# Performance work log

Hardware: AMD Instinct MI355X
Metric: run time of the kernel (lower is better)

## Reference

```python
import jax, jax.numpy as jnp
import numpy as np

N_E = 8192
E_DIM = 256
BETA = 0.25
SIGMA = 0.1


def setup_inputs() -> dict:
    key = jax.random.key(0)
    kz, ke = jax.random.split(key)
    z = jax.random.normal(kz, (16, 256, 32, 32), dtype=jnp.float32)
    # torch init: uniform(-1/n_e, 1/n_e)
    emb = jax.random.uniform(ke, (N_E, E_DIM), minval=-1.0 / N_E, maxval=1.0 / N_E, dtype=jnp.float32)
    return {"z": z, "emb": emb}


def _vq_forward(z, emb, beta=BETA, sigma=SIGMA):
    b, c, h, w = z.shape  # c == e_dim
    z_bhwc = jnp.transpose(z, (0, 2, 3, 1))  # b h w c
    zf = z_bhwc.reshape(-1, c)  # [b*h*w, c]

    # d[i, n] = ||zf_i||^2 + ||e_n||^2 - 2 zf_i . e_n
    e2 = jnp.sum(emb ** 2, axis=1)  # [n_e]
    d = jnp.sum(zf ** 2, axis=1, keepdims=True) + e2 - 2.0 * (zf @ emb.T)  # [bhw, n_e]

    # codebook-codebook pairwise distances
    d1 = e2[:, None] + e2[None, :] - 2.0 * (emb @ emb.T)  # [n_e, n_e]
    # torch.kthvalue(d1, 2, 0): 2nd smallest along dim 0, per column
    min_dist = jnp.sort(d1, axis=0)[1]  # [n_e]
    total_min_distance = jnp.sum(min_dist)
    codebookvariance = jnp.std(min_dist, ddof=1)  # torch.std is unbiased

    min_encoding_indices = jnp.argmin(d, axis=1)  # [bhw]
    # d[range, argmin] == row-wise min
    distances = jnp.min(d, axis=1).reshape(b, h, w)
    # rbf: exp(-(d^2).mean(axis=1) / (2*sigma^2)) -> [b, w]
    distances = jnp.exp(-jnp.mean(distances ** 2, axis=1) / (2.0 * sigma ** 2))

    z_q = jnp.take(emb, min_encoding_indices, axis=0).reshape(b, h, w, c)

    sg = jax.lax.stop_gradient
    # legacy=True branch
    loss = (jnp.mean((sg(z_q) - z_bhwc) ** 2)
            + beta * jnp.mean((z_q - sg(z_bhwc)) ** 2)
            - total_min_distance)

    # straight-through estimator
    z_q = z_bhwc + sg(z_q - z_bhwc)
    z_q_bchw = jnp.transpose(z_q, (0, 3, 1, 2))  # b c h w (contiguous)
    # torch .view(b, h*w, e_dim) on contiguous bchw buffer: raw reshape
    z_flattened1 = z_q_bchw.reshape(b, h * w, c)

    return (z_q_bchw, loss, distances, min_encoding_indices,
            z_flattened1, codebookvariance, total_min_distance)


def reference(z, emb):
    return _vq_forward(z, emb)
```

## Files before the change

kernel.cpp:

```cpp
#include <hip/hip_runtime.h>
#include <stdint.h>

#define N_E   8192
#define EDIM  256
#define NB    16
#define HH    32
#define WW    32
#define HW    1024
#define NI    16384
#define NELEM 4194304

#define MARGIN    2.5e-4f
#define MARGIN_D1 2e-8f
#define ITEM_CAP  262144

#define O_ZQ   0
#define O_LOSS 4194304
#define O_DIST 4194305
#define O_IDX  4194817
#define O_ZFL  4211201
#define O_CBV  8405505
#define O_TMD  8405506

#define WS_PMIN  0
#define WS_IDX   131072
#define WS_DMIN  196608
#define WS_E2    262144
#define WS_Z2    294912
#define WS_MSE   360448
#define WS_CNT   360456
#define WS_MIND  360512
#define WS_ZA    1048576
#define WS_EB    9437184
#define WS_M     13631488
#define WS_ITEMS 30408704

typedef __attribute__((ext_vector_type(8))) short bf16x8;
typedef __attribute__((ext_vector_type(4))) float f32x4;

__device__ __forceinline__ short f2bf(float f) {
    unsigned u = __float_as_uint(f);
    u += 0x7fffu + ((u >> 16) & 1u);
    return (short)(u >> 16);
}

__global__ void k_init(unsigned long long* __restrict__ pmin, double* __restrict__ mse,
                       int* __restrict__ cnt) {
    int t = blockIdx.x * 256 + threadIdx.x;
    if (t < NI) pmin[t] = 0xFFFFFFFFFFFFFFFFull;
    if (t == 0) { *mse = 0.0; *cnt = 0; }
}

__global__ void k_e2(const float* __restrict__ emb, float* __restrict__ e2) {
    int row  = blockIdx.x * 4 + (threadIdx.x >> 6);
    int lane = threadIdx.x & 63;
    float4 v = *reinterpret_cast<const float4*>(emb + (size_t)row * EDIM + lane * 4);
    float s = v.x * v.x + v.y * v.y + v.z * v.z + v.w * v.w;
    #pragma unroll
    for (int m = 32; m; m >>= 1) s += __shfl_xor(s, m);
    if (lane == 0) e2[row] = s;
}

__global__ void k_z2(const float* __restrict__ z, float* __restrict__ z2) {
    int i = blockIdx.x * 256 + threadIdx.x;
    int b = i >> 10, hw = i & 1023;
    const float* p = z + (size_t)b * EDIM * HW + hw;
    float s = 0.f;
    #pragma unroll 8
    for (int c = 0; c < EDIM; ++c) { float v = p[(size_t)c * HW]; s += v * v; }
    z2[i] = s;
}

__global__ void k_convert_z(const float* __restrict__ z, bf16x8* __restrict__ zA) {
    __shared__ float lds[64][65];
    const int t   = threadIdx.x;
    const int hw0 = blockIdx.x * 64;
    const int c0  = blockIdx.y * 64;
    const int b   = blockIdx.z;
    #pragma unroll
    for (int cc = 0; cc < 4; ++cc) {
        const int cl = cc * 16 + (t >> 4);
        const float4 v = *reinterpret_cast<const float4*>(
            z + ((size_t)(b * 256 + c0 + cl) << 10) + hw0 + (t & 15) * 4);
        lds[cl][(t & 15) * 4 + 0] = v.x; lds[cl][(t & 15) * 4 + 1] = v.y;
        lds[cl][(t & 15) * 4 + 2] = v.z; lds[cl][(t & 15) * 4 + 3] = v.w;
    }
    __syncthreads();
    const int hl = t & 63;
    const int i  = b * 1024 + hw0 + hl;
    const int ig = i >> 4, r = i & 15;
    #pragma unroll
    for (int half = 0; half < 2; ++half) {
        const int kqi = (t >> 6) + half * 4;
        const int kq  = (c0 >> 3) + kqi;
        bf16x8 o;
        #pragma unroll
        for (int j = 0; j < 8; ++j) o[j] = f2bf(lds[kqi * 8 + j][hl]);
        zA[(ig * 32 + kq) * 16 + r] = o;
    }
}

__global__ void k_convert_e(const float* __restrict__ emb, bf16x8* __restrict__ eB) {
    const int t  = threadIdx.x;
    const int kq = t & 31;
    const int n  = blockIdx.x * 8 + (t >> 5);
    const float4 u = *reinterpret_cast<const float4*>(emb + (size_t)n * EDIM + kq * 8);
    const float4 v = *reinterpret_cast<const float4*>(emb + (size_t)n * EDIM + kq * 8 + 4);
    bf16x8 o;
    o[0] = f2bf(u.x); o[1] = f2bf(u.y); o[2] = f2bf(u.z); o[3] = f2bf(u.w);
    o[4] = f2bf(v.x); o[5] = f2bf(v.y); o[6] = f2bf(v.z); o[7] = f2bf(v.w);
    eB[((n >> 4) * 32 + kq) * 16 + (n & 15)] = o;
}

__launch_bounds__(256, 2)
__global__ void k_cand(const bf16x8* __restrict__ zA, const bf16x8* __restrict__ eB,
                       const float* __restrict__ e2, float* __restrict__ m) {
    const int t = threadIdx.x;
    const int w = t >> 6, l = t & 63;
    const int lo16 = l & 15, hi4 = l >> 4;
    const int iblk = blockIdx.x, chunk = blockIdx.y;
    const int ig0 = (iblk * 128 + w * 32) >> 4;

    bf16x8 a[2][8];
    #pragma unroll
    for (int ig = 0; ig < 2; ++ig)
        #pragma unroll
        for (int st = 0; st < 8; ++st)
            a[ig][st] = zA[((ig0 + ig) * 32 + st * 4 + hi4) * 16 + lo16];

    for (int ns = 0; ns < 8; ++ns) {
        const int n0 = chunk * 1024 + ns * 128;
        f32x4 acc[2][8];
        #pragma unroll
        for (int ig = 0; ig < 2; ++ig)
            #pragma unroll
            for (int cg = 0; cg < 8; ++cg) acc[ig][cg] = (f32x4){0.f, 0.f, 0.f, 0.f};
        float e2v[8];
        #pragma unroll
        for (int cg = 0; cg < 8; ++cg) e2v[cg] = e2[n0 + cg * 16 + lo16];

        #pragma unroll
        for (int st = 0; st < 8; ++st) {
            #pragma unroll
            for (int cg = 0; cg < 8; ++cg) {
                const bf16x8 b = eB[(((n0 >> 4) + cg) * 32 + st * 4 + hi4) * 16 + lo16];
                acc[0][cg] = __builtin_amdgcn_mfma_f32_16x16x32_bf16(a[0][st], b, acc[0][cg], 0, 0, 0);
                acc[1][cg] = __builtin_amdgcn_mfma_f32_16x16x32_bf16(a[1][st], b, acc[1][cg], 0, 0, 0);
            }
        }
        #pragma unroll
        for (int ig = 0; ig < 2; ++ig) {
            #pragma unroll
            for (int reg = 0; reg < 4; ++reg) {
                const int row = iblk * 128 + w * 32 + ig * 16 + hi4 * 4 + reg;
                #pragma unroll
                for (int gp = 0; gp < 4; ++gp) {
                    float v = fminf(fmaf(-2.f, acc[ig][2 * gp][reg],     e2v[2 * gp]),
                                    fmaf(-2.f, acc[ig][2 * gp + 1][reg], e2v[2 * gp + 1]));
                    v = fminf(v, __shfl_xor(v, 1));
                    v = fminf(v, __shfl_xor(v, 2));
                    v = fminf(v, __shfl_xor(v, 4));
                    v = fminf(v, __shfl_xor(v, 8));
                    if (lo16 == gp) m[row * 256 + chunk * 32 + ns * 4 + gp] = v;
                }
            }
        }
    }
}

__launch_bounds__(256, 2)
__global__ void k_cand_d1(const bf16x8* __restrict__ eB, const float* __restrict__ e2,
                          float* __restrict__ md1) {
    const int t = threadIdx.x;
    const int w = t >> 6, l = t & 63;
    const int lo16 = l & 15, hi4 = l >> 4;
    const int iblk = blockIdx.x, chunk = blockIdx.y;
    const int ig0 = (iblk * 128 + w * 32) >> 4;

    bf16x8 a[2][8];
    #pragma unroll
    for (int ig = 0; ig < 2; ++ig)
        #pragma unroll
        for (int st = 0; st < 8; ++st)
            a[ig][st] = eB[((ig0 + ig) * 32 + st * 4 + hi4) * 16 + lo16];

    for (int ns = 0; ns < 8; ++ns) {
        const int n0 = chunk * 1024 + ns * 128;
        f32x4 acc[2][8];
        #pragma unroll
        for (int ig = 0; ig < 2; ++ig)
            #pragma unroll
            for (int cg = 0; cg < 8; ++cg) acc[ig][cg] = (f32x4){0.f, 0.f, 0.f, 0.f};
        float e2v[8];
        #pragma unroll
        for (int cg = 0; cg < 8; ++cg) e2v[cg] = e2[n0 + cg * 16 + lo16];

        #pragma unroll
        for (int st = 0; st < 8; ++st) {
            #pragma unroll
            for (int cg = 0; cg < 8; ++cg) {
                const bf16x8 b = eB[(((n0 >> 4) + cg) * 32 + st * 4 + hi4) * 16 + lo16];
                acc[0][cg] = __builtin_amdgcn_mfma_f32_16x16x32_bf16(a[0][st], b, acc[0][cg], 0, 0, 0);
                acc[1][cg] = __builtin_amdgcn_mfma_f32_16x16x32_bf16(a[1][st], b, acc[1][cg], 0, 0, 0);
            }
        }
        #pragma unroll
        for (int ig = 0; ig < 2; ++ig) {
            #pragma unroll
            for (int reg = 0; reg < 4; ++reg) {
                const int row = iblk * 128 + w * 32 + ig * 16 + hi4 * 4 + reg;
                #pragma unroll
                for (int gp = 0; gp < 4; ++gp) {
                    float v = fminf(fmaf(-2.f, acc[ig][2 * gp][reg],     e2v[2 * gp]),
                                    fmaf(-2.f, acc[ig][2 * gp + 1][reg], e2v[2 * gp + 1]));
                    v = fminf(v, __shfl_xor(v, 1));
                    v = fminf(v, __shfl_xor(v, 2));
                    v = fminf(v, __shfl_xor(v, 4));
                    v = fminf(v, __shfl_xor(v, 8));
                    if (lo16 == gp) md1[row * 256 + chunk * 32 + ns * 4 + gp] = v;
                }
            }
        }
    }
}

__global__ void k_select(const float* __restrict__ m, int* __restrict__ cnt,
                         unsigned* __restrict__ items) {
    const int t = threadIdx.x;
    const int row = blockIdx.x * 4 + (t >> 6);
    const int l = t & 63;
    const float4 mv = reinterpret_cast<const float4*>(m + (size_t)row * 256)[l];
    float v = fminf(fminf(mv.x, mv.y), fminf(mv.z, mv.w));
    #pragma unroll
    for (int o = 32; o; o >>= 1) v = fminf(v, __shfl_xor(v, o));
    const float thr = v + MARGIN;
    if (mv.x <= thr) { int p = atomicAdd(cnt, 1); if (p < ITEM_CAP) items[p] = (row << 8) | (l * 4 + 0); }
    if (mv.y <= thr) { int p = atomicAdd(cnt, 1); if (p < ITEM_CAP) items[p] = (row << 8) | (l * 4 + 1); }
    if (mv.z <= thr) { int p = atomicAdd(cnt, 1); if (p < ITEM_CAP) items[p] = (row << 8) | (l * 4 + 2); }
    if (mv.w <= thr) { int p = atomicAdd(cnt, 1); if (p < ITEM_CAP) items[p] = (row << 8) | (l * 4 + 3); }
}

__global__ void k_rescore(const float* __restrict__ z, const float* __restrict__ emb,
                          const float* __restrict__ z2, const float* __restrict__ e2,
                          const int* __restrict__ cnt, const unsigned* __restrict__ items,
                          unsigned long long* __restrict__ pmin) {
    const int t = threadIdx.x;
    const int l = t & 63;
    const int wid = blockIdx.x * 4 + (t >> 6);
    int n_items = *cnt; if (n_items > ITEM_CAP) n_items = ITEM_CAP;
    for (int it = wid; it < n_items; it += 16384) {
        const unsigned item = items[it];
        const int row = item >> 8, g = item & 255;
        const int n = g * 32 + (l & 31);
        const int half = l >> 5;
        const float* zp = z + ((size_t)(row >> 10) << 18) + (row & 1023) + (size_t)(half * 128) * HW;
        const float* ep = emb + (size_t)n * EDIM + half * 128;
        float acc = 0.f;
        #pragma unroll 8
        for (int c = 0; c < 128; ++c) acc = fmaf(zp[(size_t)c * HW], ep[c], acc);
        acc += __shfl_xor(acc, 32);
        const float t0 = z2[row] + e2[n];
        const float d  = fmaf(-2.f, acc, t0);
        unsigned long long pk = ((unsigned long long)__float_as_uint(d) << 32) | (unsigned)n;
        #pragma unroll
        for (int o = 1; o < 64; o <<= 1) {
            const unsigned long long op = __shfl_xor(pk, o);
            if (op < pk) pk = op;
        }
        if (l == 0) atomicMin(&pmin[row], pk);
    }
}

__global__ void k_d1_final(const float* __restrict__ emb, const float* __restrict__ e2,
                           const float* __restrict__ md1, float* __restrict__ mind) {
    const int t = threadIdx.x, l = t & 63;
    const int n = blockIdx.x * 4 + (t >> 6);
    const float4 mv = reinterpret_cast<const float4*>(md1 + (size_t)n * 256)[l];
    const float lo1 = fminf(mv.x, mv.y), hi1 = fmaxf(mv.x, mv.y);
    const float lo2 = fminf(mv.z, mv.w), hi2 = fmaxf(mv.z, mv.w);
    float a1 = fminf(lo1, lo2);
    float a2 = fminf(fmaxf(lo1, lo2), fminf(hi1, hi2));
    #pragma unroll
    for (int o = 1; o < 64; o <<= 1) {
        const float o1 = __shfl_xor(a1, o), o2 = __shfl_xor(a2, o);
        const float n1 = fminf(a1, o1);
        const float n2 = fminf(fmaxf(a1, o1), fminf(a2, o2));
        a1 = n1; a2 = n2;
    }
    const float thr = a2 + MARGIN_D1;
    const float e2n = e2[n];
    const float* np = emb + (size_t)n * EDIM;
    float b1 = 3.4e38f, b2 = 3.4e38f;
    const float slot[4] = {mv.x, mv.y, mv.z, mv.w};
    #pragma unroll
    for (int s = 0; s < 4; ++s) {
        unsigned long long mask = __ballot(slot[s] <= thr);
        while (mask) {
            const int src = __builtin_ctzll(mask); mask &= mask - 1;
            const int g = src * 4 + s;
            const int mm = g * 32 + (l & 31);
            const float* ep = emb + (size_t)mm * EDIM;
            float acc = 0.f;
            #pragma unroll 8
            for (int c = 0; c < EDIM; ++c) acc = fmaf(ep[c], np[c], acc);
            float dv = (e2[mm] + e2n) - 2.0f * acc;
            if (l >= 32) dv = 3.4e38f;
            if (dv < b1) { b2 = b1; b1 = dv; }
            else if (dv < b2) { b2 = dv; }
        }
    }
    #pragma unroll
    for (int o = 1; o < 64; o <<= 1) {
        const float o1 = __shfl_xor(b1, o), o2 = __shfl_xor(b2, o);
        const float n1 = fminf(b1, o1);
        const float n2 = fminf(fmaxf(b1, o1), fminf(b2, o2));
        b1 = n1; b2 = n2;
    }
    if (l == 0) mind[n] = b2;
}

__global__ void k_unpack(const unsigned long long* __restrict__ pmin,
                         int* __restrict__ idxi, float* __restrict__ dmin,
                         float* __restrict__ out_idx) {
    int i = blockIdx.x * 256 + threadIdx.x;
    unsigned long long p = pmin[i];
    int idx  = (int)(p & 0xFFFFFFFFull);
    idxi[i]  = idx;
    dmin[i]  = __uint_as_float((unsigned)(p >> 32));
    out_idx[i] = (float)idx;
}

__global__ void k_epilogue(const float* __restrict__ z, const float* __restrict__ emb,
                           const int* __restrict__ idxi,
                           float* __restrict__ out_zq, float* __restrict__ out_zfl,
                           double* __restrict__ mse) {
    const int j4 = blockIdx.x * 256 + threadIdx.x;
    const int j  = j4 * 4;
    const int b  = j >> 18;
    const int c  = (j >> 10) & 255;
    const int hw = j & 1023;
    const int ib = (b << 10) + hw;
    const float4 zv = *reinterpret_cast<const float4*>(z + j);
    const float q0 = emb[(size_t)idxi[ib + 0] * EDIM + c];
    const float q1 = emb[(size_t)idxi[ib + 1] * EDIM + c];
    const float q2 = emb[(size_t)idxi[ib + 2] * EDIM + c];
    const float q3 = emb[(size_t)idxi[ib + 3] * EDIM + c];
    const float d0 = q0 - zv.x, d1 = q1 - zv.y, d2 = q2 - zv.z, d3 = q3 - zv.w;
    const float4 st = {zv.x + d0, zv.y + d1, zv.z + d2, zv.w + d3};
    *reinterpret_cast<float4*>(out_zq + j) = st;
    out_zfl[j + 0] = st.x; out_zfl[j + 1] = st.y; out_zfl[j + 2] = st.z; out_zfl[j + 3] = st.w;

    double s = (double)(d0 * d0) + (double)(d1 * d1) + (double)(d2 * d2) + (double)(d3 * d3);
    #pragma unroll
    for (int m = 32; m; m >>= 1) s += __shfl_down(s, m);
    __shared__ double part[4];
    if ((threadIdx.x & 63) == 0) part[threadIdx.x >> 6] = s;
    __syncthreads();
    if (threadIdx.x == 0) atomicAdd(mse, part[0] + part[1] + part[2] + part[3]);
}

__global__ void k_distances(const float* __restrict__ dmin, float* __restrict__ out_d) {
    int t = threadIdx.x;
    int b = t >> 5, w = t & 31;
    float s = 0.f;
    #pragma unroll
    for (int h = 0; h < HH; ++h) {
        float d = dmin[(b << 10) + (h << 5) + w];
        s += d * d;
    }
    float mean = s * (1.0f / 32.0f);
    out_d[t] = expf(-mean / 0.02f);
}

__global__ void k_finalize(const float* __restrict__ mind, const double* __restrict__ mse,
                           float* __restrict__ out) {
    const int t = threadIdx.x;
    double s = 0.0, ss = 0.0;
    for (int n = t; n < N_E; n += 256) {
        const double v = (double)mind[n];
        s += v; ss += v * v;
    }
    #pragma unroll
    for (int m = 32; m; m >>= 1) { s += __shfl_down(s, m); ss += __shfl_down(ss, m); }
    __shared__ double rs[4], rss[4];
    if ((t & 63) == 0) { rs[t >> 6] = s; rss[t >> 6] = ss; }
    __syncthreads();
    if (t == 0) {
        const double S  = rs[0] + rs[1] + rs[2] + rs[3];
        const double SS = rss[0] + rss[1] + rss[2] + rss[3];
        const float tmd = (float)S;
        double var = (SS - S * S / (double)N_E) / (double)(N_E - 1);
        if (var < 0.0) var = 0.0;
        const float cbv = (float)sqrt(var);
        const float m1  = (float)(*mse / (double)NELEM);
        const float lossf = m1 + 0.25f * m1 - tmd;
        out[O_LOSS] = lossf;
        out[O_CBV]  = cbv;
        out[O_TMD]  = tmd;
    }
}

extern "C" void kernel_launch(void* const* d_in, const int* in_sizes, int n_in,
                              void* d_out, int out_size, void* d_ws, size_t ws_size,
                              hipStream_t stream) {
    const float* z   = (const float*)d_in[0];
    const float* emb = (const float*)d_in[1];
    float* out = (float*)d_out;
    char*  ws  = (char*)d_ws;

    unsigned long long* pmin = (unsigned long long*)(ws + WS_PMIN);
    int*      idxi  = (int*)    (ws + WS_IDX);
    float*    dmin  = (float*)  (ws + WS_DMIN);
    float*    e2    = (float*)  (ws + WS_E2);
    float*    z2    = (float*)  (ws + WS_Z2);
    double*   mse   = (double*) (ws + WS_MSE);
    int*      cnt   = (int*)    (ws + WS_CNT);
    float*    mind  = (float*)  (ws + WS_MIND);
    bf16x8*   zA    = (bf16x8*) (ws + WS_ZA);
    bf16x8*   eB    = (bf16x8*) (ws + WS_EB);
    float*    marr  = (float*)  (ws + WS_M);
    unsigned* items = (unsigned*)(ws + WS_ITEMS);

    k_init     <<<64,   256, 0, stream>>>(pmin, mse, cnt);
    k_e2       <<<2048, 256, 0, stream>>>(emb, e2);
    k_z2       <<<64,   256, 0, stream>>>(z, z2);
    k_convert_z<<<dim3(16, 4, 16), 256, 0, stream>>>(z, zA);
    k_convert_e<<<1024, 256, 0, stream>>>(emb, eB);
    k_cand     <<<dim3(128, 8), 256, 0, stream>>>(zA, eB, e2, marr);
    k_select   <<<4096, 256, 0, stream>>>(marr, cnt, items);
    k_rescore  <<<4096, 256, 0, stream>>>(z, emb, z2, e2, cnt, items, pmin);
    k_cand_d1  <<<dim3(64, 8), 256, 0, stream>>>(eB, e2, marr);
    k_d1_final <<<2048, 256, 0, stream>>>(emb, e2, marr, mind);
    k_unpack   <<<64,   256, 0, stream>>>(pmin, idxi, dmin, out + O_IDX);
    k_epilogue <<<4096, 256, 0, stream>>>(z, emb, idxi, out + O_ZQ, out + O_ZFL, mse);
    k_distances<<<1,    512, 0, stream>>>(dmin, out + O_DIST);
    k_finalize <<<1,    256, 0, stream>>>(mind, mse, out);
}
```

Before: 1.165 ms.

## Coarsen candidate groups to 128 codes and rescore per row without atomics

The bf16 candidate kernels now reduce each 128-code group to a single min, so the candidate array shrinks from 256 to 64 floats per row. The separate select kernel, its global atomic counter and the item list are removed. A per-row wavefront thresholds its own groups with a ballot and rescores each selected group exactly in fp32, two codes per lane, then writes the row minimum directly, dropping the atomicMin and the pmin initialisation. The codebook second-nearest pass is restructured the same way with a widened margin. Coarser groups mean each selected group costs more exact FP32 work and more groups may pass the threshold, trading extra rescoring for fewer launches, less memory traffic and no atomics.

```diff
diff --git a/kernel.cpp b/kernel.cpp
--- a/kernel.cpp
+++ b/kernel.cpp
@@ -12,7 +12,6 @@
 
 #define MARGIN    2.5e-4f
 #define MARGIN_D1 2e-8f
-#define ITEM_CAP  262144
 
 #define O_ZQ   0
 #define O_LOSS 4194304
@@ -28,12 +27,11 @@
 #define WS_E2    262144
 #define WS_Z2    294912
 #define WS_MSE   360448
-#define WS_CNT   360456
 #define WS_MIND  360512
 #define WS_ZA    1048576
 #define WS_EB    9437184
-#define WS_M     13631488
-#define WS_ITEMS 30408704
+#define WS_M128  13631488
+#define WS_MD1   17825792
 
 typedef __attribute__((ext_vector_type(8))) short bf16x8;
 typedef __attribute__((ext_vector_type(4))) float f32x4;
@@ -44,11 +42,8 @@
     return (short)(u >> 16);
 }
 
-__global__ void k_init(unsigned long long* __restrict__ pmin, double* __restrict__ mse,
-                       int* __restrict__ cnt) {
-    int t = blockIdx.x * 256 + threadIdx.x;
-    if (t < NI) pmin[t] = 0xFFFFFFFFFFFFFFFFull;
-    if (t == 0) { *mse = 0.0; *cnt = 0; }
+__global__ void k_init(double* __restrict__ mse) {
+    if (threadIdx.x == 0) *mse = 0.0;
 }
 
 __global__ void k_e2(const float* __restrict__ emb, float* __restrict__ e2) {
@@ -114,7 +109,7 @@
 
 __launch_bounds__(256, 2)
 __global__ void k_cand(const bf16x8* __restrict__ zA, const bf16x8* __restrict__ eB,
-                       const float* __restrict__ e2, float* __restrict__ m) {
+                       const float* __restrict__ e2, float* __restrict__ m128) {
     const int t = threadIdx.x;
     const int w = t >> 6, l = t & 63;
     const int lo16 = l & 15, hi4 = l >> 4;
@@ -152,16 +147,17 @@
         for (int ig = 0; ig < 2; ++ig) {
             #pragma unroll
             for (int reg = 0; reg < 4; ++reg) {
-                const int row = iblk * 128 + w * 32 + ig * 16 + hi4 * 4 + reg;
+                float v = fmaf(-2.f, acc[ig][0][reg], e2v[0]);
                 #pragma unroll
-                for (int gp = 0; gp < 4; ++gp) {
-                    float v = fminf(fmaf(-2.f, acc[ig][2 * gp][reg],     e2v[2 * gp]),
-                                    fmaf(-2.f, acc[ig][2 * gp + 1][reg], e2v[2 * gp + 1]));
-                    v = fminf(v, __shfl_xor(v, 1));
-                    v = fminf(v, __shfl_xor(v, 2));
-                    v = fminf(v, __shfl_xor(v, 4));
-                    v = fminf(v, __shfl_xor(v, 8));
-                    if (lo16 == gp) m[row * 256 + chunk * 32 + ns * 4 + gp] = v;
+                for (int cg = 1; cg < 8; ++cg)
+                    v = fminf(v, fmaf(-2.f, acc[ig][cg][reg], e2v[cg]));
+                v = fminf(v, __shfl_xor(v, 1));
+                v = fminf(v, __shfl_xor(v, 2));
+                v = fminf(v, __shfl_xor(v, 4));
+                v = fminf(v, __shfl_xor(v, 8));
+                if (lo16 == ns) {
+                    const int row = iblk * 128 + w * 32 + ig * 16 + hi4 * 4 + reg;
+                    m128[row * 64 + chunk * 8 + ns] = v;
                 }
             }
         }
@@ -208,78 +204,79 @@
         for (int ig = 0; ig < 2; ++ig) {
             #pragma unroll
             for (int reg = 0; reg < 4; ++reg) {
-                const int row = iblk * 128 + w * 32 + ig * 16 + hi4 * 4 + reg;
+                float v = fmaf(-2.f, acc[ig][0][reg], e2v[0]);
                 #pragma unroll
-                for (int gp = 0; gp < 4; ++gp) {
-                    float v = fminf(fmaf(-2.f, acc[ig][2 * gp][reg],     e2v[2 * gp]),
-                                    fmaf(-2.f, acc[ig][2 * gp + 1][reg], e2v[2 * gp + 1]));
-                    v = fminf(v, __shfl_xor(v, 1));
-                    v = fminf(v, __shfl_xor(v, 2));
-                    v = fminf(v, __shfl_xor(v, 4));
-                    v = fminf(v, __shfl_xor(v, 8));
-                    if (lo16 == gp) md1[row * 256 + chunk * 32 + ns * 4 + gp] = v;
+                for (int cg = 1; cg < 8; ++cg)
+                    v = fminf(v, fmaf(-2.f, acc[ig][cg][reg], e2v[cg]));
+                v = fminf(v, __shfl_xor(v, 1));
+                v = fminf(v, __shfl_xor(v, 2));
+                v = fminf(v, __shfl_xor(v, 4));
+                v = fminf(v, __shfl_xor(v, 8));
+                if (lo16 == ns) {
+                    const int row = iblk * 128 + w * 32 + ig * 16 + hi4 * 4 + reg;
+                    md1[row * 64 + chunk * 8 + ns] = v;
                 }
             }
         }
     }
 }
 
-__global__ void k_select(const float* __restrict__ m, int* __restrict__ cnt,
-                         unsigned* __restrict__ items) {
-    const int t = threadIdx.x;
+__global__ void k_rescore_row(const float* __restrict__ z, const float* __restrict__ emb,
+                              const float* __restrict__ z2, const float* __restrict__ e2,
+                              const float* __restrict__ m128,
+                              unsigned long long* __restrict__ pmin) {
+    const int t = threadIdx.x, l = t & 63;
     const int row = blockIdx.x * 4 + (t >> 6);
-    const int l = t & 63;
-    const float4 mv = reinterpret_cast<const float4*>(m + (size_t)row * 256)[l];
-    float v = fminf(fminf(mv.x, mv.y), fminf(mv.z, mv.w));
-    #pragma unroll
-    for (int o = 32; o; o >>= 1) v = fminf(v, __shfl_xor(v, o));
-    const float thr = v + MARGIN;
-    if (mv.x <= thr) { int p = atomicAdd(cnt, 1); if (p < ITEM_CAP) items[p] = (row << 8) | (l * 4 + 0); }
-    if (mv.y <= thr) { int p = atomicAdd(cnt, 1); if (p < ITEM_CAP) items[p] = (row << 8) | (l * 4 + 1); }
-    if (mv.z <= thr) { int p = atomicAdd(cnt, 1); if (p < ITEM_CAP) items[p] = (row << 8) | (l * 4 + 2); }
-    if (mv.w <= thr) { int p = atomicAdd(cnt, 1); if (p < ITEM_CAP) items[p] = (row << 8) | (l * 4 + 3); }
-}
-
-__global__ void k_rescore(const float* __restrict__ z, const float* __restrict__ emb,
-                          const float* __restrict__ z2, const float* __restrict__ e2,
-                          const int* __restrict__ cnt, const unsigned* __restrict__ items,
-                          unsigned long long* __restrict__ pmin) {
-    const int t = threadIdx.x;
-    const int l = t & 63;
-    const int wid = blockIdx.x * 4 + (t >> 6);
-    int n_items = *cnt; if (n_items > ITEM_CAP) n_items = ITEM_CAP;
-    for (int it = wid; it < n_items; it += 16384) {
-        const unsigned item = items[it];
-        const int row = item >> 8, g = item & 255;
-        const int n = g * 32 + (l & 31);
-        const int half = l >> 5;
-        const float* zp = z + ((size_t)(row >> 10) << 18) + (row & 1023) + (size_t)(half * 128) * HW;
-        const float* ep = emb + (size_t)n * EDIM + half * 128;
-        float acc = 0.f;
-        #pragma unroll 8
-        for (int c = 0; c < 128; ++c) acc = fmaf(zp[(size_t)c * HW], ep[c], acc);
-        acc += __shfl_xor(acc, 32);
-        const float t0 = z2[row] + e2[n];
-        const float d  = fmaf(-2.f, acc, t0);
-        unsigned long long pk = ((unsigned long long)__float_as_uint(d) << 32) | (unsigned)n;
-        #pragma unroll
-        for (int o = 1; o < 64; o <<= 1) {
-            const unsigned long long op = __shfl_xor(pk, o);
-            if (op < pk) pk = op;
-        }
-        if (l == 0) atomicMin(&pmin[row], pk);
-    }
+    const float v = m128[row * 64 + l];
+    float mn = v;
+    #pragma unroll
+    for (int o = 1; o < 64; o <<= 1) mn = fminf(mn, __shfl_xor(mn, o));
+    unsigned long long mm = __ballot(v <= mn + MARGIN);
+
+    const float* zp = z + ((size_t)(row >> 10) << 18) + (row & 1023);
+    const float z2r = z2[row];
+    unsigned long long best = 0xFFFFFFFFFFFFFFFFull;
+    while (mm) {
+        const int g = __builtin_ctzll(mm); mm &= mm - 1;
+        const int n = g * 128 + l * 2;
+        const float* ep0 = emb + (size_t)n * EDIM;
+        const float* ep1 = ep0 + EDIM;
+        float a0l = 0.f, a0h = 0.f, a1l = 0.f, a1h = 0.f;
+        #pragma unroll 4
+        for (int c = 0; c < 128; ++c) {
+            const float zc = zp[(size_t)c << 10];
+            a0l = fmaf(zc, ep0[c], a0l);
+            a1l = fmaf(zc, ep1[c], a1l);
+        }
+        #pragma unroll 4
+        for (int c = 128; c < 256; ++c) {
+            const float zc = zp[(size_t)c << 10];
+            a0h = fmaf(zc, ep0[c], a0h);
+            a1h = fmaf(zc, ep1[c], a1h);
+        }
+        const float d0 = fmaf(-2.f, a0l + a0h, z2r + e2[n]);
+        const float d1 = fmaf(-2.f, a1l + a1h, z2r + e2[n + 1]);
+        const unsigned long long p0 =
+            ((unsigned long long)__float_as_uint(d0) << 32) | (unsigned)n;
+        const unsigned long long p1 =
+            ((unsigned long long)__float_as_uint(d1) << 32) | (unsigned)(n + 1);
+        const unsigned long long pl = p0 < p1 ? p0 : p1;
+        if (pl < best) best = pl;
+    }
+    #pragma unroll
+    for (int o = 1; o < 64; o <<= 1) {
+        const unsigned long long ob = __shfl_xor(best, o);
+        if (ob < best) best = ob;
+    }
+    if (l == 0) pmin[row] = best;
 }
 
 __global__ void k_d1_final(const float* __restrict__ emb, const float* __restrict__ e2,
                            const float* __restrict__ md1, float* __restrict__ mind) {
     const int t = threadIdx.x, l = t & 63;
     const int n = blockIdx.x * 4 + (t >> 6);
-    const float4 mv = reinterpret_cast<const float4*>(md1 + (size_t)n * 256)[l];
-    const float lo1 = fminf(mv.x, mv.y), hi1 = fmaxf(mv.x, mv.y);
-    const float lo2 = fminf(mv.z, mv.w), hi2 = fmaxf(mv.z, mv.w);
-    float a1 = fminf(lo1, lo2);
-    float a2 = fminf(fmaxf(lo1, lo2), fminf(hi1, hi2));
+    const float v = md1[n * 64 + l];
+    float a1 = v, a2 = 3.4e38f;
     #pragma unroll
     for (int o = 1; o < 64; o <<= 1) {
         const float o1 = __shfl_xor(a1, o), o2 = __shfl_xor(a2, o);
@@ -287,27 +284,29 @@
         const float n2 = fminf(fmaxf(a1, o1), fminf(a2, o2));
         a1 = n1; a2 = n2;
     }
-    const float thr = a2 + MARGIN_D1;
+    const float thr = a2 + 2.0f * MARGIN_D1;
+    unsigned long long mm = __ballot(v <= thr);
     const float e2n = e2[n];
     const float* np = emb + (size_t)n * EDIM;
     float b1 = 3.4e38f, b2 = 3.4e38f;
-    const float slot[4] = {mv.x, mv.y, mv.z, mv.w};
-    #pragma unroll
-    for (int s = 0; s < 4; ++s) {
-        unsigned long long mask = __ballot(slot[s] <= thr);
-        while (mask) {
-            const int src = __builtin_ctzll(mask); mask &= mask - 1;
-            const int g = src * 4 + s;
-            const int mm = g * 32 + (l & 31);
-            const float* ep = emb + (size_t)mm * EDIM;
-            float acc = 0.f;
-            #pragma unroll 8
-            for (int c = 0; c < EDIM; ++c) acc = fmaf(ep[c], np[c], acc);
-            float dv = (e2[mm] + e2n) - 2.0f * acc;
-            if (l >= 32) dv = 3.4e38f;
-            if (dv < b1) { b2 = b1; b1 = dv; }
-            else if (dv < b2) { b2 = dv; }
-        }
+    while (mm) {
+        const int g = __builtin_ctzll(mm); mm &= mm - 1;
+        const int m0 = g * 128 + l * 2;
+        const float* p0 = emb + (size_t)m0 * EDIM;
+        const float* p1 = p0 + EDIM;
+        float c0 = 0.f, c1 = 0.f;
+        #pragma unroll 8
+        for (int c = 0; c < EDIM; ++c) {
+            const float nc = np[c];
+            c0 = fmaf(p0[c], nc, c0);
+            c1 = fmaf(p1[c], nc, c1);
+        }
+        const float d0 = (e2[m0] + e2n) - 2.0f * c0;
+        const float d1 = (e2[m0 + 1] + e2n) - 2.0f * c1;
+        const float lo = fminf(d0, d1), hi = fmaxf(d0, d1);
+        const float nb1 = fminf(b1, lo);
+        const float nb2 = fminf(fmaxf(b1, lo), fminf(b2, hi));
+        b1 = nb1; b2 = nb2;
     }
     #pragma unroll
     for (int o = 1; o < 64; o <<= 1) {
@@ -414,25 +413,23 @@
     float*    e2    = (float*)  (ws + WS_E2);
     float*    z2    = (float*)  (ws + WS_Z2);
     double*   mse   = (double*) (ws + WS_MSE);
-    int*      cnt   = (int*)    (ws + WS_CNT);
     float*    mind  = (float*)  (ws + WS_MIND);
     bf16x8*   zA    = (bf16x8*) (ws + WS_ZA);
     bf16x8*   eB    = (bf16x8*) (ws + WS_EB);
-    float*    marr  = (float*)  (ws + WS_M);
-    unsigned* items = (unsigned*)(ws + WS_ITEMS);
-
-    k_init     <<<64,   256, 0, stream>>>(pmin, mse, cnt);
-    k_e2       <<<2048, 256, 0, stream>>>(emb, e2);
-    k_z2       <<<64,   256, 0, stream>>>(z, z2);
-    k_convert_z<<<dim3(16, 4, 16), 256, 0, stream>>>(z, zA);
-    k_convert_e<<<1024, 256, 0, stream>>>(emb, eB);
-    k_cand     <<<dim3(128, 8), 256, 0, stream>>>(zA, eB, e2, marr);
-    k_select   <<<4096, 256, 0, stream>>>(marr, cnt, items);
-    k_rescore  <<<4096, 256, 0, stream>>>(z, emb, z2, e2, cnt, items, pmin);
-    k_cand_d1  <<<dim3(64, 8), 256, 0, stream>>>(eB, e2, marr);
-    k_d1_final <<<2048, 256, 0, stream>>>(emb, e2, marr, mind);
-    k_unpack   <<<64,   256, 0, stream>>>(pmin, idxi, dmin, out + O_IDX);
-    k_epilogue <<<4096, 256, 0, stream>>>(z, emb, idxi, out + O_ZQ, out + O_ZFL, mse);
-    k_distances<<<1,    512, 0, stream>>>(dmin, out + O_DIST);
-    k_finalize <<<1,    256, 0, stream>>>(mind, mse, out);
-}
+    float*    m128  = (float*)  (ws + WS_M128);
+    float*    md1   = (float*)  (ws + WS_MD1);
+
+    k_init       <<<1,    64,  0, stream>>>(mse);
+    k_e2         <<<2048, 256, 0, stream>>>(emb, e2);
+    k_z2         <<<64,   256, 0, stream>>>(z, z2);
+    k_convert_z  <<<dim3(16, 4, 16), 256, 0, stream>>>(z, zA);
+    k_convert_e  <<<1024, 256, 0, stream>>>(emb, eB);
+    k_cand       <<<dim3(128, 8), 256, 0, stream>>>(zA, eB, e2, m128);
+    k_rescore_row<<<4096, 256, 0, stream>>>(z, emb, z2, e2, m128, pmin);
+    k_cand_d1    <<<dim3(64, 8), 256, 0, stream>>>(eB, e2, md1);
+    k_d1_final   <<<2048, 256, 0, stream>>>(emb, e2, md1, mind);
+    k_unpack     <<<64,   256, 0, stream>>>(pmin, idxi, dmin, out + O_IDX);
+    k_epilogue   <<<4096, 256, 0, stream>>>(z, emb, idxi, out + O_ZQ, out + O_ZFL, mse);
+    k_distances  <<<1,    512, 0, stream>>>(dmin, out + O_DIST);
+    k_finalize   <<<1,    256, 0, stream>>>(mind, mse, out);
+}
```

Measured after the change: 2.155 ms. +85.0%, slower.

## Use split-bf16 triple MFMA with in-kernel top-2 tracking, drop select/rescore passes

Applied to the files above, without the earlier changes.

Both GEMM kernels now split each fp32 operand into bf16 high and low parts and issue three MFMAs (hi*hi, hi*lo, lo*hi) per tile, giving near-fp32 accuracy. Each thread tracks a packed (distance key, index) top-2 per row in registers and writes only two candidates per row per chunk, instead of dumping per-group minima. The atomic-based select and rescore pipeline is replaced by small merge kernels that rescore just the top-2 candidates exactly in fp32. This cuts candidate-buffer traffic and atomics, and the A fragments are now reloaded per step instead of held in registers. The cost is three times the MFMA work, and the reduced candidate set relies on the split-bf16 precision to keep the true minimum.

```diff
diff --git a/kernel.cpp b/kernel.cpp
--- a/kernel.cpp
+++ b/kernel.cpp
@@ -10,9 +10,7 @@
 #define NI    16384
 #define NELEM 4194304
 
-#define MARGIN    2.5e-4f
-#define MARGIN_D1 2e-8f
-#define ITEM_CAP  262144
+#define MARGIN_D1 1e-9f
 
 #define O_ZQ   0
 #define O_LOSS 4194304
@@ -22,18 +20,18 @@
 #define O_CBV  8405505
 #define O_TMD  8405506
 
-#define WS_PMIN  0
-#define WS_IDX   131072
-#define WS_DMIN  196608
-#define WS_E2    262144
-#define WS_Z2    294912
-#define WS_MSE   360448
-#define WS_CNT   360456
-#define WS_MIND  360512
-#define WS_ZA    1048576
-#define WS_EB    9437184
-#define WS_M     13631488
-#define WS_ITEMS 30408704
+#define WS_IDX   0x0
+#define WS_DMIN  0x20000
+#define WS_E2    0x40000
+#define WS_Z2    0x50000
+#define WS_MSE   0x60000
+#define WS_MIND  0x61000
+#define WS_PZ    0x70000
+#define WS_PD1   0x270000
+#define WS_ZAH   0x400000
+#define WS_ZAL   0xC00000
+#define WS_EBH   0x1400000
+#define WS_EBL   0x1800000
 
 typedef __attribute__((ext_vector_type(8))) short bf16x8;
 typedef __attribute__((ext_vector_type(4))) float f32x4;
@@ -43,12 +41,30 @@
     u += 0x7fffu + ((u >> 16) & 1u);
     return (short)(u >> 16);
 }
-
-__global__ void k_init(unsigned long long* __restrict__ pmin, double* __restrict__ mse,
-                       int* __restrict__ cnt) {
-    int t = blockIdx.x * 256 + threadIdx.x;
-    if (t < NI) pmin[t] = 0xFFFFFFFFFFFFFFFFull;
-    if (t == 0) { *mse = 0.0; *cnt = 0; }
+__device__ __forceinline__ float bf2f(short h) {
+    return __uint_as_float(((unsigned)(unsigned short)h) << 16);
+}
+__device__ __forceinline__ unsigned keyf(float f) {
+    unsigned b = __float_as_uint(f);
+    return (b & 0x80000000u) ? ~b : (b | 0x80000000u);
+}
+__device__ __forceinline__ float unkeyf(unsigned k) {
+    return (k & 0x80000000u) ? __uint_as_float(k ^ 0x80000000u) : __uint_as_float(~k);
+}
+__device__ __forceinline__ void ins2(unsigned long long& a1, unsigned long long& a2,
+                                     unsigned long long v) {
+    if (v < a1) { a2 = a1; a1 = v; } else if (v < a2) { a2 = v; }
+}
+__device__ __forceinline__ void mrg2(unsigned long long& a1, unsigned long long& a2,
+                                     unsigned long long b1, unsigned long long b2) {
+    unsigned long long n1 = a1 < b1 ? a1 : b1;
+    unsigned long long mx = a1 < b1 ? b1 : a1;
+    unsigned long long mn = a2 < b2 ? a2 : b2;
+    a1 = n1; a2 = mx < mn ? mx : mn;
+}
+
+__global__ void k_init(double* __restrict__ mse) {
+    if (threadIdx.x == 0) *mse = 0.0;
 }
 
 __global__ void k_e2(const float* __restrict__ emb, float* __restrict__ e2) {
@@ -71,7 +87,8 @@
     z2[i] = s;
 }
 
-__global__ void k_convert_z(const float* __restrict__ z, bf16x8* __restrict__ zA) {
+__global__ void k_convert_z(const float* __restrict__ z,
+                            bf16x8* __restrict__ zAh, bf16x8* __restrict__ zAl) {
     __shared__ float lds[64][65];
     const int t   = threadIdx.x;
     const int hw0 = blockIdx.x * 64;
@@ -93,40 +110,61 @@
     for (int half = 0; half < 2; ++half) {
         const int kqi = (t >> 6) + half * 4;
         const int kq  = (c0 >> 3) + kqi;
-        bf16x8 o;
-        #pragma unroll
-        for (int j = 0; j < 8; ++j) o[j] = f2bf(lds[kqi * 8 + j][hl]);
-        zA[(ig * 32 + kq) * 16 + r] = o;
-    }
-}
-
-__global__ void k_convert_e(const float* __restrict__ emb, bf16x8* __restrict__ eB) {
+        bf16x8 oh, ol;
+        #pragma unroll
+        for (int j = 0; j < 8; ++j) {
+            const float f = lds[kqi * 8 + j][hl];
+            const short h = f2bf(f);
+            oh[j] = h;
+            ol[j] = f2bf(f - bf2f(h));
+        }
+        zAh[(ig * 32 + kq) * 16 + r] = oh;
+        zAl[(ig * 32 + kq) * 16 + r] = ol;
+    }
+}
+
+__global__ void k_convert_e(const float* __restrict__ emb,
+                            bf16x8* __restrict__ eBh, bf16x8* __restrict__ eBl) {
     const int t  = threadIdx.x;
     const int kq = t & 31;
     const int n  = blockIdx.x * 8 + (t >> 5);
     const float4 u = *reinterpret_cast<const float4*>(emb + (size_t)n * EDIM + kq * 8);
     const float4 v = *reinterpret_cast<const float4*>(emb + (size_t)n * EDIM + kq * 8 + 4);
-    bf16x8 o;
-    o[0] = f2bf(u.x); o[1] = f2bf(u.y); o[2] = f2bf(u.z); o[3] = f2bf(u.w);
-    o[4] = f2bf(v.x); o[5] = f2bf(v.y); o[6] = f2bf(v.z); o[7] = f2bf(v.w);
-    eB[((n >> 4) * 32 + kq) * 16 + (n & 15)] = o;
+    const float fv[8] = {u.x, u.y, u.z, u.w, v.x, v.y, v.z, v.w};
+    bf16x8 oh, ol;
+    #pragma unroll
+    for (int j = 0; j < 8; ++j) {
+        const short h = f2bf(fv[j]);
+        oh[j] = h;
+        ol[j] = f2bf(fv[j] - bf2f(h));
+    }
+    eBh[((n >> 4) * 32 + kq) * 16 + (n & 15)] = oh;
+    eBl[((n >> 4) * 32 + kq) * 16 + (n & 15)] = ol;
 }
 
 __launch_bounds__(256, 2)
-__global__ void k_cand(const bf16x8* __restrict__ zA, const bf16x8* __restrict__ eB,
-                       const float* __restrict__ e2, float* __restrict__ m) {
+__global__ void k_cand(const bf16x8* __restrict__ zAh, const bf16x8* __restrict__ zAl,
+                       const bf16x8* __restrict__ eBh, const bf16x8* __restrict__ eBl,
+                       const float* __restrict__ z2, const float* __restrict__ e2,
+                       unsigned long long* __restrict__ pz) {
     const int t = threadIdx.x;
     const int w = t >> 6, l = t & 63;
     const int lo16 = l & 15, hi4 = l >> 4;
     const int iblk = blockIdx.x, chunk = blockIdx.y;
     const int ig0 = (iblk * 128 + w * 32) >> 4;
 
-    bf16x8 a[2][8];
+    float z2r[2][4];
     #pragma unroll
     for (int ig = 0; ig < 2; ++ig)
         #pragma unroll
-        for (int st = 0; st < 8; ++st)
-            a[ig][st] = zA[((ig0 + ig) * 32 + st * 4 + hi4) * 16 + lo16];
+        for (int reg = 0; reg < 4; ++reg)
+            z2r[ig][reg] = z2[iblk * 128 + w * 32 + ig * 16 + hi4 * 4 + reg];
+
+    unsigned long long t1[2][4], t2[2][4];
+    #pragma unroll
+    for (int ig = 0; ig < 2; ++ig)
+        #pragma unroll
+        for (int reg = 0; reg < 4; ++reg) { t1[ig][reg] = ~0ull; t2[ig][reg] = ~0ull; }
 
     for (int ns = 0; ns < 8; ++ns) {
         const int n0 = chunk * 1024 + ns * 128;
@@ -135,54 +173,77 @@
         for (int ig = 0; ig < 2; ++ig)
             #pragma unroll
             for (int cg = 0; cg < 8; ++cg) acc[ig][cg] = (f32x4){0.f, 0.f, 0.f, 0.f};
+
+        #pragma unroll
+        for (int st = 0; st < 8; ++st) {
+            const bf16x8 ah0 = zAh[((ig0 + 0) * 32 + st * 4 + hi4) * 16 + lo16];
+            const bf16x8 ah1 = zAh[((ig0 + 1) * 32 + st * 4 + hi4) * 16 + lo16];
+            const bf16x8 al0 = zAl[((ig0 + 0) * 32 + st * 4 + hi4) * 16 + lo16];
+            const bf16x8 al1 = zAl[((ig0 + 1) * 32 + st * 4 + hi4) * 16 + lo16];
+            #pragma unroll
+            for (int cg = 0; cg < 8; ++cg) {
+                const bf16x8 bh = eBh[(((n0 >> 4) + cg) * 32 + st * 4 + hi4) * 16 + lo16];
+                const bf16x8 bl = eBl[(((n0 >> 4) + cg) * 32 + st * 4 + hi4) * 16 + lo16];
+                acc[0][cg] = __builtin_amdgcn_mfma_f32_16x16x32_bf16(ah0, bh, acc[0][cg], 0, 0, 0);
+                acc[0][cg] = __builtin_amdgcn_mfma_f32_16x16x32_bf16(ah0, bl, acc[0][cg], 0, 0, 0);
+                acc[0][cg] = __builtin_amdgcn_mfma_f32_16x16x32_bf16(al0, bh, acc[0][cg], 0, 0, 0);
+                acc[1][cg] = __builtin_amdgcn_mfma_f32_16x16x32_bf16(ah1, bh, acc[1][cg], 0, 0, 0);
+                acc[1][cg] = __builtin_amdgcn_mfma_f32_16x16x32_bf16(ah1, bl, acc[1][cg], 0, 0, 0);
+                acc[1][cg] = __builtin_amdgcn_mfma_f32_16x16x32_bf16(al1, bh, acc[1][cg], 0, 0, 0);
+            }
+        }
         float e2v[8];
         #pragma unroll
         for (int cg = 0; cg < 8; ++cg) e2v[cg] = e2[n0 + cg * 16 + lo16];
-
-        #pragma unroll
-        for (int st = 0; st < 8; ++st) {
-            #pragma unroll
-            for (int cg = 0; cg < 8; ++cg) {
-                const bf16x8 b = eB[(((n0 >> 4) + cg) * 32 + st * 4 + hi4) * 16 + lo16];
-                acc[0][cg] = __builtin_amdgcn_mfma_f32_16x16x32_bf16(a[0][st], b, acc[0][cg], 0, 0, 0);
-                acc[1][cg] = __builtin_amdgcn_mfma_f32_16x16x32_bf16(a[1][st], b, acc[1][cg], 0, 0, 0);
-            }
-        }
         #pragma unroll
         for (int ig = 0; ig < 2; ++ig) {
             #pragma unroll
             for (int reg = 0; reg < 4; ++reg) {
+                #pragma unroll
+                for (int cg = 0; cg < 8; ++cg) {
+                    const float d = fmaf(-2.f, acc[ig][cg][reg], z2r[ig][reg] + e2v[cg]);
+                    const unsigned long long pk =
+                        ((unsigned long long)keyf(d) << 32) | (unsigned)(n0 + cg * 16 + lo16);
+                    ins2(t1[ig][reg], t2[ig][reg], pk);
+                }
+            }
+        }
+    }
+    #pragma unroll
+    for (int ig = 0; ig < 2; ++ig) {
+        #pragma unroll
+        for (int reg = 0; reg < 4; ++reg) {
+            unsigned long long a1 = t1[ig][reg], a2 = t2[ig][reg];
+            #pragma unroll
+            for (int o = 1; o < 16; o <<= 1) {
+                const unsigned long long b1 = __shfl_xor(a1, o);
+                const unsigned long long b2 = __shfl_xor(a2, o);
+                mrg2(a1, a2, b1, b2);
+            }
+            if (lo16 == 0) {
                 const int row = iblk * 128 + w * 32 + ig * 16 + hi4 * 4 + reg;
-                #pragma unroll
-                for (int gp = 0; gp < 4; ++gp) {
-                    float v = fminf(fmaf(-2.f, acc[ig][2 * gp][reg],     e2v[2 * gp]),
-                                    fmaf(-2.f, acc[ig][2 * gp + 1][reg], e2v[2 * gp + 1]));
-                    v = fminf(v, __shfl_xor(v, 1));
-                    v = fminf(v, __shfl_xor(v, 2));
-                    v = fminf(v, __shfl_xor(v, 4));
-                    v = fminf(v, __shfl_xor(v, 8));
-                    if (lo16 == gp) m[row * 256 + chunk * 32 + ns * 4 + gp] = v;
-                }
+                pz[(row * 8 + chunk) * 2 + 0] = a1;
+                pz[(row * 8 + chunk) * 2 + 1] = a2;
             }
         }
     }
 }
 
 __launch_bounds__(256, 2)
-__global__ void k_cand_d1(const bf16x8* __restrict__ eB, const float* __restrict__ e2,
-                          float* __restrict__ md1) {
+__global__ void k_cand_d1(const bf16x8* __restrict__ eBh, const bf16x8* __restrict__ eBl,
+                          const float* __restrict__ e2,
+                          unsigned long long* __restrict__ pd1) {
     const int t = threadIdx.x;
     const int w = t >> 6, l = t & 63;
     const int lo16 = l & 15, hi4 = l >> 4;
     const int iblk = blockIdx.x, chunk = blockIdx.y;
     const int ig0 = (iblk * 128 + w * 32) >> 4;
 
-    bf16x8 a[2][8];
+    unsigned long long t1[2][4], t2[2][4];
     #pragma unroll
     for (int ig = 0; ig < 2; ++ig)
         #pragma unroll
-        for (int st = 0; st < 8; ++st)
-            a[ig][st] = eB[((ig0 + ig) * 32 + st * 4 + hi4) * 16 + lo16];
+        for (int reg = 0; reg < 4; ++reg) { t1[ig][reg] = ~0ull; t2[ig][reg] = ~0ull; }
 
     for (int ns = 0; ns < 8; ++ns) {
         const int n0 = chunk * 1024 + ns * 128;
@@ -191,143 +252,127 @@
         for (int ig = 0; ig < 2; ++ig)
             #pragma unroll
             for (int cg = 0; cg < 8; ++cg) acc[ig][cg] = (f32x4){0.f, 0.f, 0.f, 0.f};
+
+        #pragma unroll
+        for (int st = 0; st < 8; ++st) {
+            const bf16x8 ah0 = eBh[((ig0 + 0) * 32 + st * 4 + hi4) * 16 + lo16];
+            const bf16x8 ah1 = eBh[((ig0 + 1) * 32 + st * 4 + hi4) * 16 + lo16];
+            const bf16x8 al0 = eBl[((ig0 + 0) * 32 + st * 4 + hi4) * 16 + lo16];
+            const bf16x8 al1 = eBl[((ig0 + 1) * 32 + st * 4 + hi4) * 16 + lo16];
+            #pragma unroll
+            for (int cg = 0; cg < 8; ++cg) {
+                const bf16x8 bh = eBh[(((n0 >> 4) + cg) * 32 + st * 4 + hi4) * 16 + lo16];
+                const bf16x8 bl = eBl[(((n0 >> 4) + cg) * 32 + st * 4 + hi4) * 16 + lo16];
+                acc[0][cg] = __builtin_amdgcn_mfma_f32_16x16x32_bf16(ah0, bh, acc[0][cg], 0, 0, 0);
+                acc[0][cg] = __builtin_amdgcn_mfma_f32_16x16x32_bf16(ah0, bl, acc[0][cg], 0, 0, 0);
+                acc[0][cg] = __builtin_amdgcn_mfma_f32_16x16x32_bf16(al0, bh, acc[0][cg], 0, 0, 0);
+                acc[1][cg] = __builtin_amdgcn_mfma_f32_16x16x32_bf16(ah1, bh, acc[1][cg], 0, 0, 0);
+                acc[1][cg] = __builtin_amdgcn_mfma_f32_16x16x32_bf16(ah1, bl, acc[1][cg], 0, 0, 0);
+                acc[1][cg] = __builtin_amdgcn_mfma_f32_16x16x32_bf16(al1, bh, acc[1][cg], 0, 0, 0);
+            }
+        }
         float e2v[8];
         #pragma unroll
         for (int cg = 0; cg < 8; ++cg) e2v[cg] = e2[n0 + cg * 16 + lo16];
-
-        #pragma unroll
-        for (int st = 0; st < 8; ++st) {
-            #pragma unroll
-            for (int cg = 0; cg < 8; ++cg) {
-                const bf16x8 b = eB[(((n0 >> 4) + cg) * 32 + st * 4 + hi4) * 16 + lo16];
-                acc[0][cg] = __builtin_amdgcn_mfma_f32_16x16x32_bf16(a[0][st], b, acc[0][cg], 0, 0, 0);
-                acc[1][cg] = __builtin_amdgcn_mfma_f32_16x16x32_bf16(a[1][st], b, acc[1][cg], 0, 0, 0);
-            }
-        }
         #pragma unroll
         for (int ig = 0; ig < 2; ++ig) {
             #pragma unroll
             for (int reg = 0; reg < 4; ++reg) {
+                #pragma unroll
+                for (int cg = 0; cg < 8; ++cg) {
+                    const float q = fmaf(-2.f, acc[ig][cg][reg], e2v[cg]);
+                    const unsigned long long pk =
+                        ((unsigned long long)keyf(q) << 32) | (unsigned)(n0 + cg * 16 + lo16);
+                    ins2(t1[ig][reg], t2[ig][reg], pk);
+                }
+            }
+        }
+    }
+    #pragma unroll
+    for (int ig = 0; ig < 2; ++ig) {
+        #pragma unroll
+        for (int reg = 0; reg < 4; ++reg) {
+            unsigned long long a1 = t1[ig][reg], a2 = t2[ig][reg];
+            #pragma unroll
+            for (int o = 1; o < 16; o <<= 1) {
+                const unsigned long long b1 = __shfl_xor(a1, o);
+                const unsigned long long b2 = __shfl_xor(a2, o);
+                mrg2(a1, a2, b1, b2);
+            }
+            if (lo16 == 0) {
                 const int row = iblk * 128 + w * 32 + ig * 16 + hi4 * 4 + reg;
-                #pragma unroll
-                for (int gp = 0; gp < 4; ++gp) {
-                    float v = fminf(fmaf(-2.f, acc[ig][2 * gp][reg],     e2v[2 * gp]),
-                                    fmaf(-2.f, acc[ig][2 * gp + 1][reg], e2v[2 * gp + 1]));
-                    v = fminf(v, __shfl_xor(v, 1));
-                    v = fminf(v, __shfl_xor(v, 2));
-                    v = fminf(v, __shfl_xor(v, 4));
-                    v = fminf(v, __shfl_xor(v, 8));
-                    if (lo16 == gp) md1[row * 256 + chunk * 32 + ns * 4 + gp] = v;
-                }
-            }
-        }
-    }
-}
-
-__global__ void k_select(const float* __restrict__ m, int* __restrict__ cnt,
-                         unsigned* __restrict__ items) {
-    const int t = threadIdx.x;
-    const int row = blockIdx.x * 4 + (t >> 6);
-    const int l = t & 63;
-    const float4 mv = reinterpret_cast<const float4*>(m + (size_t)row * 256)[l];
-    float v = fminf(fminf(mv.x, mv.y), fminf(mv.z, mv.w));
-    #pragma unroll
-    for (int o = 32; o; o >>= 1) v = fminf(v, __shfl_xor(v, o));
-    const float thr = v + MARGIN;
-    if (mv.x <= thr) { int p = atomicAdd(cnt, 1); if (p < ITEM_CAP) items[p] = (row << 8) | (l * 4 + 0); }
-    if (mv.y <= thr) { int p = atomicAdd(cnt, 1); if (p < ITEM_CAP) items[p] = (row << 8) | (l * 4 + 1); }
-    if (mv.z <= thr) { int p = atomicAdd(cnt, 1); if (p < ITEM_CAP) items[p] = (row << 8) | (l * 4 + 2); }
-    if (mv.w <= thr) { int p = atomicAdd(cnt, 1); if (p < ITEM_CAP) items[p] = (row << 8) | (l * 4 + 3); }
-}
-
-__global__ void k_rescore(const float* __restrict__ z, const float* __restrict__ emb,
-                          const float* __restrict__ z2, const float* __restrict__ e2,
-                          const int* __restrict__ cnt, const unsigned* __restrict__ items,
-                          unsigned long long* __restrict__ pmin) {
-    const int t = threadIdx.x;
-    const int l = t & 63;
-    const int wid = blockIdx.x * 4 + (t >> 6);
-    int n_items = *cnt; if (n_items > ITEM_CAP) n_items = ITEM_CAP;
-    for (int it = wid; it < n_items; it += 16384) {
-        const unsigned item = items[it];
-        const int row = item >> 8, g = item & 255;
-        const int n = g * 32 + (l & 31);
-        const int half = l >> 5;
-        const float* zp = z + ((size_t)(row >> 10) << 18) + (row & 1023) + (size_t)(half * 128) * HW;
-        const float* ep = emb + (size_t)n * EDIM + half * 128;
-        float acc = 0.f;
-        #pragma unroll 8
-        for (int c = 0; c < 128; ++c) acc = fmaf(zp[(size_t)c * HW], ep[c], acc);
-        acc += __shfl_xor(acc, 32);
-        const float t0 = z2[row] + e2[n];
-        const float d  = fmaf(-2.f, acc, t0);
-        unsigned long long pk = ((unsigned long long)__float_as_uint(d) << 32) | (unsigned)n;
-        #pragma unroll
-        for (int o = 1; o < 64; o <<= 1) {
-            const unsigned long long op = __shfl_xor(pk, o);
-            if (op < pk) pk = op;
-        }
-        if (l == 0) atomicMin(&pmin[row], pk);
-    }
-}
-
-__global__ void k_d1_final(const float* __restrict__ emb, const float* __restrict__ e2,
-                           const float* __restrict__ md1, float* __restrict__ mind) {
+                pd1[(row * 8 + chunk) * 2 + 0] = a1;
+                pd1[(row * 8 + chunk) * 2 + 1] = a2;
+            }
+        }
+    }
+}
+
+__global__ void k_zmerge(const float* __restrict__ z, const float* __restrict__ emb,
+                         const float* __restrict__ z2, const float* __restrict__ e2,
+                         const unsigned long long* __restrict__ pz,
+                         int* __restrict__ idxi, float* __restrict__ dmin,
+                         float* __restrict__ out_idx) {
     const int t = threadIdx.x, l = t & 63;
-    const int n = blockIdx.x * 4 + (t >> 6);
-    const float4 mv = reinterpret_cast<const float4*>(md1 + (size_t)n * 256)[l];
-    const float lo1 = fminf(mv.x, mv.y), hi1 = fmaxf(mv.x, mv.y);
-    const float lo2 = fminf(mv.z, mv.w), hi2 = fmaxf(mv.z, mv.w);
-    float a1 = fminf(lo1, lo2);
-    float a2 = fminf(fmaxf(lo1, lo2), fminf(hi1, hi2));
-    #pragma unroll
-    for (int o = 1; o < 64; o <<= 1) {
-        const float o1 = __shfl_xor(a1, o), o2 = __shfl_xor(a2, o);
-        const float n1 = fminf(a1, o1);
-        const float n2 = fminf(fmaxf(a1, o1), fminf(a2, o2));
-        a1 = n1; a2 = n2;
-    }
-    const float thr = a2 + MARGIN_D1;
+    const int row = blockIdx.x * 64 + (t >> 6) * 16 + (l >> 2);
+    const int cs = (l >> 1) & 1, hf = l & 1;
+    unsigned long long a1 = ~0ull, a2 = ~0ull;
+    #pragma unroll
+    for (int k = 0; k < 4; ++k)
+        ins2(a1, a2, pz[row * 16 + (l & 3) * 4 + k]);
+    #pragma unroll
+    for (int o = 1; o < 4; o <<= 1) {
+        const unsigned long long b1 = __shfl_xor(a1, o);
+        const unsigned long long b2 = __shfl_xor(a2, o);
+        mrg2(a1, a2, b1, b2);
+    }
+    const int n = (unsigned)(cs ? a2 : a1);
+    const float* zp = z + ((size_t)(row >> 10) << 18) + (row & 1023);
+    const float* ep = emb + (size_t)n * EDIM;
+    float acc = 0.f;
+    #pragma unroll 8
+    for (int c = 0; c < 128; ++c) {
+        const int cc = hf * 128 + c;
+        acc = fmaf(zp[(size_t)cc << 10], ep[cc], acc);
+    }
+    const float total = acc + __shfl_xor(acc, 1);
+    const float d = fmaf(-2.f, total, z2[row] + e2[n]);
+    unsigned long long pk = ((unsigned long long)__float_as_uint(d) << 32) | (unsigned)n;
+    const unsigned long long op = __shfl_xor(pk, 2);
+    if (op < pk) pk = op;
+    if ((l & 3) == 0) {
+        const int ni = (int)(pk & 0xFFFFFFFFull);
+        idxi[row] = ni;
+        dmin[row] = __uint_as_float((unsigned)(pk >> 32));
+        out_idx[row] = (float)ni;
+    }
+}
+
+__global__ void k_d1merge(const float* __restrict__ emb, const float* __restrict__ e2,
+                          const unsigned long long* __restrict__ pd1,
+                          float* __restrict__ mind) {
+    const int n = blockIdx.x * 256 + threadIdx.x;
+    unsigned long long w1 = ~0ull, w2 = ~0ull;
+    unsigned long long ent[16];
+    #pragma unroll
+    for (int e = 0; e < 16; ++e) { ent[e] = pd1[n * 16 + e]; ins2(w1, w2, ent[e]); }
+    const float thr = unkeyf((unsigned)(w2 >> 32)) + MARGIN_D1;
     const float e2n = e2[n];
     const float* np = emb + (size_t)n * EDIM;
     float b1 = 3.4e38f, b2 = 3.4e38f;
-    const float slot[4] = {mv.x, mv.y, mv.z, mv.w};
-    #pragma unroll
-    for (int s = 0; s < 4; ++s) {
-        unsigned long long mask = __ballot(slot[s] <= thr);
-        while (mask) {
-            const int src = __builtin_ctzll(mask); mask &= mask - 1;
-            const int g = src * 4 + s;
-            const int mm = g * 32 + (l & 31);
-            const float* ep = emb + (size_t)mm * EDIM;
-            float acc = 0.f;
-            #pragma unroll 8
-            for (int c = 0; c < EDIM; ++c) acc = fmaf(ep[c], np[c], acc);
-            float dv = (e2[mm] + e2n) - 2.0f * acc;
-            if (l >= 32) dv = 3.4e38f;
-            if (dv < b1) { b2 = b1; b1 = dv; }
-            else if (dv < b2) { b2 = dv; }
-        }
-    }
-    #pragma unroll
-    for (int o = 1; o < 64; o <<= 1) {
-        const float o1 = __shfl_xor(b1, o), o2 = __shfl_xor(b2, o);
-        const float n1 = fminf(b1, o1);
-        const float n2 = fminf(fmaxf(b1, o1), fminf(b2, o2));
-        b1 = n1; b2 = n2;
-    }
-    if (l == 0) mind[n] = b2;
-}
-
-__global__ void k_unpack(const unsigned long long* __restrict__ pmin,
-                         int* __restrict__ idxi, float* __restrict__ dmin,
-                         float* __restrict__ out_idx) {
-    int i = blockIdx.x * 256 + threadIdx.x;
-    unsigned long long p = pmin[i];
-    int idx  = (int)(p & 0xFFFFFFFFull);
-    idxi[i]  = idx;
-    dmin[i]  = __uint_as_float((unsigned)(p >> 32));
-    out_idx[i] = (float)idx;
+    #pragma unroll 1
+    for (int e = 0; e < 16; ++e) {
+        const float af = unkeyf((unsigned)(ent[e] >> 32));
+        if (af > thr) continue;
+        const int m = (unsigned)ent[e];
+        const float* ep = emb + (size_t)m * EDIM;
+        float acc = 0.f;
+        #pragma unroll 8
+        for (int c = 0; c < EDIM; ++c) acc = fmaf(ep[c], np[c], acc);
+        const float dv = (e2[m] + e2n) - 2.0f * acc;
+        if (dv < b1) { b2 = b1; b1 = dv; } else if (dv < b2) { b2 = dv; }
+    }
+    mind[n] = b2;
 }
 
 __global__ void k_epilogue(const float* __restrict__ z, const float* __restrict__ emb,
@@ -408,30 +453,28 @@
     float* out = (float*)d_out;
     char*  ws  = (char*)d_ws;
 
-    unsigned long long* pmin = (unsigned long long*)(ws + WS_PMIN);
-    int*      idxi  = (int*)    (ws + WS_IDX);
-    float*    dmin  = (float*)  (ws + WS_DMIN);
-    float*    e2    = (float*)  (ws + WS_E2);
-    float*    z2    = (float*)  (ws + WS_Z2);
-    double*   mse   = (double*) (ws + WS_MSE);
-    int*      cnt   = (int*)    (ws + WS_CNT);
-    float*    mind  = (float*)  (ws + WS_MIND);
-    bf16x8*   zA    = (bf16x8*) (ws + WS_ZA);
-    bf16x8*   eB    = (bf16x8*) (ws + WS_EB);
-    float*    marr  = (float*)  (ws + WS_M);
-    unsigned* items = (unsigned*)(ws + WS_ITEMS);
-
-    k_init     <<<64,   256, 0, stream>>>(pmin, mse, cnt);
+    int*      idxi = (int*)    (ws + WS_IDX);
+    float*    dmin = (float*)  (ws + WS_DMIN);
+    float*    e2   = (float*)  (ws + WS_E2);
+    float*    z2   = (float*)  (ws + WS_Z2);
+    double*   mse  = (double*) (ws + WS_MSE);
+    float*    mind = (float*)  (ws + WS_MIND);
+    unsigned long long* pz  = (unsigned long long*)(ws + WS_PZ);
+    unsigned long long* pd1 = (unsigned long long*)(ws + WS_PD1);
+    bf16x8*   zAh  = (bf16x8*) (ws + WS_ZAH);
+    bf16x8*   zAl  = (bf16x8*) (ws + WS_ZAL);
+    bf16x8*   eBh  = (bf16x8*) (ws + WS_EBH);
+    bf16x8*   eBl  = (bf16x8*) (ws + WS_EBL);
+
+    k_init     <<<1,    64,  0, stream>>>(mse);
     k_e2       <<<2048, 256, 0, stream>>>(emb, e2);
     k_z2       <<<64,   256, 0, stream>>>(z, z2);
-    k_convert_z<<<dim3(16, 4, 16), 256, 0, stream>>>(z, zA);
-    k_convert_e<<<1024, 256, 0, stream>>>(emb, eB);
-    k_cand     <<<dim3(128, 8), 256, 0, stream>>>(zA, eB, e2, marr);
-    k_select   <<<4096, 256, 0, stream>>>(marr, cnt, items);
-    k_rescore  <<<4096, 256, 0, stream>>>(z, emb, z2, e2, cnt, items, pmin);
-    k_cand_d1  <<<dim3(64, 8), 256, 0, stream>>>(eB, e2, marr);
-    k_d1_final <<<2048, 256, 0, stream>>>(emb, e2, marr, mind);
-    k_unpack   <<<64,   256, 0, stream>>>(pmin, idxi, dmin, out + O_IDX);
+    k_convert_z<<<dim3(16, 4, 16), 256, 0, stream>>>(z, zAh, zAl);
+    k_convert_e<<<1024, 256, 0, stream>>>(emb, eBh, eBl);
+    k_cand     <<<dim3(128, 8), 256, 0, stream>>>(zAh, zAl, eBh, eBl, z2, e2, pz);
+    k_cand_d1  <<<dim3(64, 8),  256, 0, stream>>>(eBh, eBl, e2, pd1);
+    k_zmerge   <<<256,  256, 0, stream>>>(z, emb, z2, e2, pz, idxi, dmin, out + O_IDX);
+    k_d1merge  <<<32,   256, 0, stream>>>(emb, e2, pd1, mind);
     k_epilogue <<<4096, 256, 0, stream>>>(z, emb, idxi, out + O_ZQ, out + O_ZFL, mse);
     k_distances<<<1,    512, 0, stream>>>(dmin, out + O_DIST);
     k_finalize <<<1,    256, 0, stream>>>(mind, mse, out);
```

Result: slower. 1.279 ms (+9.8%).
